# Kernel tuning notes

Hardware: AMD Instinct MI355X
Metric: run time of the kernel (lower is better)

## Reference

```python
import jax, jax.numpy as jnp
import numpy as np
from jax import lax

U, K, POOL, STRIDE, FC = 300, 19, 7, 7, 100   # num_units, filter size, maxpool, fc_size
B, L, D = 256, 1000, 4                        # batch, seq len, DNA dim
P = (L - (K - 1) - (POOL - 1) - 1) // STRIDE + 1  # post_pool_size = 140
EPS = 1e-5  # BatchNorm eps (eval mode with running stats; Dropout is identity in eval)


def setup_inputs() -> dict:
    key = jax.random.key(0)
    ks = jax.random.split(key, 24)
    rn = lambda k, shp, s=0.1: jax.random.normal(k, shp, jnp.float32) * s
    return {
        "input_seq": jax.random.normal(ks[0], (B, L, D), jnp.float32),
        # per-unit conv (groups=U on tiled input == plain Conv1d(4, U, K))
        "w_conv": rn(ks[1], (U, D, K)), "b_conv": rn(ks[2], (U,)),
        "g1": 1.0 + rn(ks[3], (U,)), "be1": rn(ks[4], (U,)),
        "m1": rn(ks[5], (U,)), "v1": 1.0 + jax.random.uniform(ks[6], (U,), jnp.float32),
        # per-unit FC1 (grouped 1x1 conv: P -> FC per unit)
        "w_fc1": rn(ks[7], (U, FC, P)), "b_fc1": rn(ks[8], (U, FC)),
        "g2": 1.0 + rn(ks[9], (U, FC)), "be2": rn(ks[10], (U, FC)),
        "m2": rn(ks[11], (U, FC)), "v2": 1.0 + jax.random.uniform(ks[12], (U, FC), jnp.float32),
        # per-unit FC2 (grouped 1x1 conv: FC -> 1 per unit)
        "w_fc2": rn(ks[13], (U, FC)), "b_fc2": rn(ks[14], (U,)),
        "g3": 1.0 + rn(ks[15], (U,)), "be3": rn(ks[16], (U,)),
        "m3": rn(ks[17], (U,)), "v3": 1.0 + jax.random.uniform(ks[18], (U,), jnp.float32),
        # final Linear(U, 1)
        "w_out": rn(ks[19], (U, 1)), "b_out": rn(ks[20], (1,)),
    }


def reference(input_seq, w_conv, b_conv, g1, be1, m1, v1, w_fc1, b_fc1,
              g2, be2, m2, v2, w_fc2, b_fc2, g3, be3, m3, v3, w_out, b_out):
    x = jnp.transpose(input_seq, (0, 2, 1))  # B,D,L
    # grouped conv on input tiled U times: every group sees the same D=4 channels,
    # so it is exactly a plain Conv1d(D, U, K).
    conv = lax.conv_general_dilated(
        x, w_conv, (1,), 'VALID', dimension_numbers=('NCH', 'OIH', 'NCH')
    ) + b_conv[None, :, None]                 # B,U,L' (L'=L-K+1)
    a = (conv - m1[None, :, None]) * (g1 / jnp.sqrt(v1 + EPS))[None, :, None] + be1[None, :, None]
    a = jnp.exp(a)
    pooled = lax.reduce_window(a, -jnp.inf, lax.max,
                               (1, 1, POOL), (1, 1, STRIDE), 'VALID')  # B,U,P
    # Flatten->Unsqueeze->grouped 1x1 conv == per-unit matmul over P
    h = jnp.einsum('bup,ufp->buf', pooled, w_fc1) + b_fc1               # B,U,FC
    h = jax.nn.relu((h - m2) * (g2 / jnp.sqrt(v2 + EPS)) + be2)
    z = jnp.einsum('buf,uf->bu', h, w_fc2) + b_fc2                      # B,U
    z = jax.nn.relu((z - m3) * (g3 / jnp.sqrt(v3 + EPS)) + be3)
    return jax.nn.sigmoid(z @ w_out + b_out)                            # B,1
```

## Files before the change

kernel.cpp:

```cpp
#include <hip/hip_runtime.h>
#include <hip/hip_bf16.h>
#include <math.h>

#define U_   300
#define K_   19
#define FC_  100
#define B_   256
#define L_   1000
#define P_   140
#define EPS_ 1e-5f
#define WLD_ 144

typedef unsigned short ushort_t;
typedef __attribute__((ext_vector_type(8)))  short short8v;
typedef __attribute__((ext_vector_type(16))) float f32x16;

__device__ __forceinline__ ushort_t f2bf(float f) {
    union { float f; unsigned u; } a; a.f = f;
    unsigned r = a.u + 0x7fffu + ((a.u >> 16) & 1u);
    return (ushort_t)(r >> 16);
}

__global__ __launch_bounds__(256, 4)
void pack_conv_k(const float* __restrict__ w_conv, const float* __restrict__ b_conv,
                 const float* __restrict__ g1, const float* __restrict__ be1,
                 const float* __restrict__ m1, const float* __restrict__ v1,
                 ushort_t* __restrict__ w_bf, float* __restrict__ o1g)
{
    const int t = blockIdx.x * 256 + threadIdx.x;
    if (t < 320 * 80) {
        const int u = t / 80, j = t - u * 80;
        float val = 0.f;
        if (u < U_ && j < 76) {
            const int tp = j >> 2;
            const int d  = j & 3;
            const float s1 = g1[u] / sqrtf(v1[u] + EPS_);
            val = w_conv[u * 76 + 19 * d + tp] * s1;
        }
        const int nt = u >> 5, r = u & 31;
        const int kc = j >> 4, rem = j & 15;
        const int half = rem >> 3, e = rem & 7;
        w_bf[nt * 2560 + kc * 512 + half * 256 + r * 8 + e] = f2bf(val);
    }
    if (t < 320) {
        float o = 0.f;
        if (t < U_) {
            const float s1 = g1[t] / sqrtf(v1[t] + EPS_);
            o = (b_conv[t] - m1[t]) * s1 + be1[t];
        }
        o1g[t] = o;
    }
}

__global__ __launch_bounds__(448, 4)
void conv_mfma_k(const float4* __restrict__ x4,
                 const ushort_t* __restrict__ w_bf,
                 const float* __restrict__ o1g,
                 ushort_t* __restrict__ pooled)
{
    __shared__ ushort_t xls[2][880];
    __shared__ ushort_t wlds[12800];
    __shared__ ushort_t stage[32][68];
    const int tid = threadIdx.x;
    const int bx  = blockIdx.x;
    const int nh  = blockIdx.y;
    const int b0  = 2 * blockIdx.z;
    const int w0  = bx * 28;
    const int l0  = w0 * 7;

    if (tid < 440) {
        const int which = (tid >= 220) ? 1 : 0;
        const int i = tid - 220 * which;
        const int gi = l0 + i;
        float4 v = make_float4(0.f, 0.f, 0.f, 0.f);
        if (gi < L_) v = x4[(size_t)(b0 + which) * L_ + gi];
        ushort4 pk4;
        pk4.x = f2bf(v.x); pk4.y = f2bf(v.y); pk4.z = f2bf(v.z); pk4.w = f2bf(v.w);
        *(ushort4*)&xls[which][4 * i] = pk4;
    }
    {
        const float4* ws = (const float4*)w_bf + nh * 1600;
        float4* wd = (float4*)wlds;
        for (int i = tid; i < 1600; i += 448) wd[i] = ws[i];
    }
    __syncthreads();

    const int lane = tid & 63;
    const int mt   = tid >> 6;
    const int half = lane >> 5;
    const int r32  = lane & 31;

    const int sreg = (r32 & 3) + 4 * (r32 >> 3);
    const int sh   = (r32 >> 2) & 1;
    const int off  = sreg < 7  ? sreg + 7 * sh
                   : sreg < 14 ? sreg + 7 + 7 * sh
                               : 28 + (sreg - 14) + 2 * sh;

    const char* xb0 = (const char*)&xls[0][0] + 8 * (28 * mt + off) + 16 * half;
    const char* xb1 = xb0 + 1760;
    const char* wl  = (const char*)wlds + 16 * lane;

    short8v aA0[5], aA1[5];
#pragma unroll
    for (int kc = 0; kc < 5; ++kc) {
        aA0[kc] = *(const short8v*)(xb0 + 32 * kc);
        aA1[kc] = *(const short8v*)(xb1 + 32 * kc);
    }

    const int dr  = tid / 7;
    const int dcc = tid - 7 * dr;
    const int dul = dr >> 1;
    const int dbl = dr & 1;

    const int p0off = 4 * mt + half;

    short8v bfr[5];
#pragma unroll
    for (int kc = 0; kc < 5; ++kc)
        bfr[kc] = *(const short8v*)(wl + kc * 1024);
    float o1u = o1g[nh * 160 + r32];

    for (int ntp = 0; ntp < 5; ++ntp) {
        const int ntn = (ntp < 4) ? ntp + 1 : ntp;
        short8v bnx[5];
#pragma unroll
        for (int kc = 0; kc < 5; ++kc)
            bnx[kc] = *(const short8v*)(wl + ntn * 5120 + kc * 1024);
        const float o1n = o1g[nh * 160 + ntn * 32 + r32];

        f32x16 acc0 = {};
        f32x16 acc1 = {};
#pragma unroll
        for (int kc = 0; kc < 5; ++kc) {
            acc0 = __builtin_amdgcn_mfma_f32_32x32x16_bf16(aA0[kc], bfr[kc], acc0, 0, 0, 0);
            acc1 = __builtin_amdgcn_mfma_f32_32x32x16_bf16(aA1[kc], bfr[kc], acc1, 0, 0, 0);
        }

        float m00 = acc0[0], m01 = acc0[7];
        float m10 = acc1[0], m11 = acc1[7];
#pragma unroll
        for (int j = 1; j < 7; ++j)  { m00 = fmaxf(m00, acc0[j]); m10 = fmaxf(m10, acc1[j]); }
#pragma unroll
        for (int j = 8; j < 14; ++j) { m01 = fmaxf(m01, acc0[j]); m11 = fmaxf(m11, acc1[j]); }

        stage[r32][p0off]          = f2bf(__expf(m00 + o1u));
        stage[r32][p0off + 2]      = f2bf(__expf(m01 + o1u));
        stage[r32][32 + p0off]     = f2bf(__expf(m10 + o1u));
        stage[r32][32 + p0off + 2] = f2bf(__expf(m11 + o1u));
        __syncthreads();

        const int ug = nh * 160 + ntp * 32 + dul;
        if (ug < U_) {
            const ushort4 st = *(const ushort4*)&stage[dul][dbl * 32 + 4 * dcc];
            *(ushort4*)&pooled[((size_t)ug * B_ + (b0 + dbl)) * P_ + w0 + 4 * dcc] = st;
        }
        __syncthreads();

#pragma unroll
        for (int kc = 0; kc < 5; ++kc) bfr[kc] = bnx[kc];
        o1u = o1n;
    }
}

__global__ __launch_bounds__(256, 3)
void fc_mfma_k(const ushort_t* __restrict__ pooled,
               const float* __restrict__ w_fc1,
               const float* __restrict__ b_fc1,
               const float* __restrict__ g2,
               const float* __restrict__ be2,
               const float* __restrict__ m2,
               const float* __restrict__ v2,
               const float* __restrict__ w_fc2,
               const float* __restrict__ b_fc2,
               const float* __restrict__ g3,
               const float* __restrict__ be3,
               const float* __restrict__ m3,
               const float* __restrict__ v3,
               float* __restrict__ zT)
{
    __shared__ ushort_t wlds[FC_ * WLD_];
    __shared__ float zred[128][33];
    const int tid  = threadIdx.x;
    const int bid = blockIdx.x;
    int u, bt;
    if (bid < 592) {
        const int r = bid & 7, k = bid >> 3;
        bt = k & 1;
        u  = (k >> 1) * 8 + r;
    } else {
        const int t = bid - 592;
        u  = 296 + (t >> 1);
        bt = t & 1;
    }

    const int lane = tid & 63;
    const int wv   = tid >> 6;
    const int half = lane >> 5;
    const int r32  = lane & 31;

    const int brow = bt * 128 + wv * 32 + r32;
    const ushort_t* __restrict__ abase =
        pooled + ((size_t)u * B_ + brow) * P_ + half * 8;
    short8v a[9];
#pragma unroll
    for (int kc = 0; kc < 9; ++kc)
        a[kc] = *(const short8v*)(abase + kc * 16);

    const float* __restrict__ wsrc = w_fc1 + (size_t)u * FC_ * P_;
    for (int idx = tid; idx < FC_ * 35; idx += 256) {
        const int f = idx / 35, j = idx - f * 35;
        const float4 v = *(const float4*)(wsrc + f * P_ + 4 * j);
        ushort4 pk;
        pk.x = f2bf(v.x); pk.y = f2bf(v.y); pk.z = f2bf(v.z); pk.w = f2bf(v.w);
        *(ushort4*)&wlds[f * WLD_ + 4 * j] = pk;
    }
    for (int idx = tid; idx < FC_ * 4; idx += 256) {
        const int f = idx >> 2, k = 140 + (idx & 3);
        wlds[f * WLD_ + k] = 0;
    }
    __syncthreads();

    const ushort_t* __restrict__ bl0 = &wlds[r32 * WLD_ + half * 8];
    const ushort_t* __restrict__ bl1 = &wlds[(32 + r32) * WLD_ + half * 8];
    const ushort_t* __restrict__ bl2 = &wlds[(64 + r32) * WLD_ + half * 8];
    const int f3c = (96 + r32 < FC_) ? (96 + r32) : (FC_ - 1);
    const ushort_t* __restrict__ bl3 = &wlds[f3c * WLD_ + half * 8];

    f32x16 acc0 = {}, acc1 = {}, acc2 = {}, acc3 = {};
#pragma unroll
    for (int kc = 0; kc < 9; ++kc) {
        const short8v b0 = *(const short8v*)(bl0 + kc * 16);
        const short8v b1 = *(const short8v*)(bl1 + kc * 16);
        const short8v b2 = *(const short8v*)(bl2 + kc * 16);
        const short8v b3 = *(const short8v*)(bl3 + kc * 16);
        acc0 = __builtin_amdgcn_mfma_f32_32x32x16_bf16(a[kc], b0, acc0, 0, 0, 0);
        acc1 = __builtin_amdgcn_mfma_f32_32x32x16_bf16(a[kc], b1, acc1, 0, 0, 0);
        acc2 = __builtin_amdgcn_mfma_f32_32x32x16_bf16(a[kc], b2, acc2, 0, 0, 0);
        acc3 = __builtin_amdgcn_mfma_f32_32x32x16_bf16(a[kc], b3, acc3, 0, 0, 0);
    }

    float s2[4], o2[4], w2[4];
#pragma unroll
    for (int n = 0; n < 4; ++n) {
        const int f = n * 32 + r32;
        if (f < FC_) {
            const int fg = u * FC_ + f;
            const float ss = g2[fg] / sqrtf(v2[fg] + EPS_);
            s2[n] = ss;
            o2[n] = (b_fc1[fg] - m2[fg]) * ss + be2[fg];
            w2[n] = w_fc2[fg];
        } else {
            s2[n] = 0.f; o2[n] = 0.f; w2[n] = 0.f;
        }
    }
#pragma unroll
    for (int rg = 0; rg < 16; ++rg) {
        const int row = (rg & 3) + 8 * (rg >> 2) + 4 * half;
        float s = fmaxf(fmaf(acc0[rg], s2[0], o2[0]), 0.f) * w2[0];
        s = fmaf(fmaxf(fmaf(acc1[rg], s2[1], o2[1]), 0.f), w2[1], s);
        s = fmaf(fmaxf(fmaf(acc2[rg], s2[2], o2[2]), 0.f), w2[2], s);
        s = fmaf(fmaxf(fmaf(acc3[rg], s2[3], o2[3]), 0.f), w2[3], s);
        zred[wv * 32 + row][r32] = s;
    }
    __syncthreads();

    if (tid < 128) {
        float s = 0.f;
#pragma unroll
        for (int j = 0; j < 32; ++j) s += zred[tid][j];
        const float s3 = g3[u] / sqrtf(v3[u] + EPS_);
        const float o3 = (b_fc2[u] - m3[u]) * s3 + be3[u];
        zT[(size_t)(bt * 128 + tid) * 304 + u] = fmaxf(fmaf(s, s3, o3), 0.f);
    }
}

__global__ __launch_bounds__(64, 8)
void out_k(const float* __restrict__ zT,
           const float* __restrict__ w_out,
           const float* __restrict__ b_out,
           float* __restrict__ out)
{
    const int lane = threadIdx.x;
    const int b    = blockIdx.x;
    const float4* zr = (const float4*)(zT + (size_t)b * 304);
    const float4* w4 = (const float4*)w_out;

    float s = 0.f;
    for (int i = lane; i < 75; i += 64) {
        const float4 z = zr[i], w = w4[i];
        s += z.x * w.x + z.y * w.y + z.z * w.z + z.w * w.w;
    }
#pragma unroll
    for (int o = 32; o > 0; o >>= 1) s += __shfl_xor(s, o);
    if (lane == 0)
        out[b] = 1.0f / (1.0f + __expf(-(s + b_out[0])));
}

extern "C" void kernel_launch(void* const* d_in, const int* in_sizes, int n_in,
                              void* d_out, int out_size, void* d_ws, size_t ws_size,
                              hipStream_t stream)
{
    const float* input_seq = (const float*)d_in[0];
    const float* w_conv    = (const float*)d_in[1];
    const float* b_conv    = (const float*)d_in[2];
    const float* g1        = (const float*)d_in[3];
    const float* be1       = (const float*)d_in[4];
    const float* m1        = (const float*)d_in[5];
    const float* v1        = (const float*)d_in[6];
    const float* w_fc1     = (const float*)d_in[7];
    const float* b_fc1     = (const float*)d_in[8];
    const float* g2        = (const float*)d_in[9];
    const float* be2       = (const float*)d_in[10];
    const float* m2        = (const float*)d_in[11];
    const float* v2        = (const float*)d_in[12];
    const float* w_fc2     = (const float*)d_in[13];
    const float* b_fc2     = (const float*)d_in[14];
    const float* g3        = (const float*)d_in[15];
    const float* be3       = (const float*)d_in[16];
    const float* m3        = (const float*)d_in[17];
    const float* v3        = (const float*)d_in[18];
    const float* w_out     = (const float*)d_in[19];
    const float* b_out     = (const float*)d_in[20];

    char* p = (char*)d_ws;
    ushort_t* pooled = (ushort_t*)p;   p += (size_t)B_ * U_ * P_ * 2;
    ushort_t* w_bf   = (ushort_t*)p;   p += 320 * 80 * 2;
    float*    o1g    = (float*)p;      p += 320 * 4;
    float*    zT     = (float*)p;      p += (size_t)B_ * 304 * 4;

    pack_conv_k<<<dim3(100), 256, 0, stream>>>(
        w_conv, b_conv, g1, be1, m1, v1, w_bf, o1g);

    conv_mfma_k<<<dim3(5, 2, 128), 448, 0, stream>>>(
        (const float4*)input_seq, w_bf, o1g, pooled);

    fc_mfma_k<<<dim3(600), 256, 0, stream>>>(
        pooled, w_fc1, b_fc1, g2, be2, m2, v2, w_fc2, b_fc2,
        g3, be3, m3, v3, zT);

    out_k<<<dim3(B_), 64, 0, stream>>>(zT, w_out, b_out, (float*)d_out);
}
```

Measured before the change: 55.77 us.

## Keep conv weights in registers and loop over batch pairs with double-buffered input

The conv kernel changes from staging a 160-unit weight slab in LDS and looping over five unit tiles to having each block hold one 32-unit weight tile in registers and loop over eight batch pairs. Input rows for the next batch pair are prefetched from global memory and written into a double-buffered LDS tile during the current iteration. This drops the large weight LDS copy and raises weight reuse per block, at the cost of fewer blocks overall and reloading input for each unit tile.

```diff
diff --git a/kernel.cpp b/kernel.cpp
--- a/kernel.cpp
+++ b/kernel.cpp
@@ -58,82 +58,77 @@
                  const float* __restrict__ o1g,
                  ushort_t* __restrict__ pooled)
 {
-    __shared__ ushort_t xls[2][880];
-    __shared__ ushort_t wlds[12800];
+    __shared__ ushort_t xls[2][2][880];
     __shared__ ushort_t stage[32][68];
     const int tid = threadIdx.x;
     const int bx  = blockIdx.x;
-    const int nh  = blockIdx.y;
-    const int b0  = 2 * blockIdx.z;
+    const int nt  = blockIdx.y;
+    const int pg  = blockIdx.z;
     const int w0  = bx * 28;
     const int l0  = w0 * 7;
-
-    if (tid < 440) {
-        const int which = (tid >= 220) ? 1 : 0;
-        const int i = tid - 220 * which;
-        const int gi = l0 + i;
-        float4 v = make_float4(0.f, 0.f, 0.f, 0.f);
-        if (gi < L_) v = x4[(size_t)(b0 + which) * L_ + gi];
-        ushort4 pk4;
-        pk4.x = f2bf(v.x); pk4.y = f2bf(v.y); pk4.z = f2bf(v.z); pk4.w = f2bf(v.w);
-        *(ushort4*)&xls[which][4 * i] = pk4;
-    }
-    {
-        const float4* ws = (const float4*)w_bf + nh * 1600;
-        float4* wd = (float4*)wlds;
-        for (int i = tid; i < 1600; i += 448) wd[i] = ws[i];
-    }
-    __syncthreads();
 
     const int lane = tid & 63;
     const int mt   = tid >> 6;
     const int half = lane >> 5;
     const int r32  = lane & 31;
+
+    const char* wgl = (const char*)w_bf + nt * 5120 + 16 * lane;
+    short8v Bf[5];
+#pragma unroll
+    for (int kc = 0; kc < 5; ++kc)
+        Bf[kc] = *(const short8v*)(wgl + kc * 1024);
+    const float o1u = o1g[nt * 32 + r32];
+
+    const int swhich = (tid >= 220) ? 1 : 0;
+    const int srow   = tid - 220 * swhich;
+    const int gi     = l0 + srow;
+
+    {
+        const int b00 = 2 * (pg * 8);
+        if (tid < 440) {
+            float4 v = make_float4(0.f, 0.f, 0.f, 0.f);
+            if (gi < L_) v = x4[(size_t)(b00 + swhich) * L_ + gi];
+            ushort4 pk4;
+            pk4.x = f2bf(v.x); pk4.y = f2bf(v.y); pk4.z = f2bf(v.z); pk4.w = f2bf(v.w);
+            *(ushort4*)&xls[0][swhich][4 * srow] = pk4;
+        }
+    }
+    __syncthreads();
 
     const int sreg = (r32 & 3) + 4 * (r32 >> 3);
     const int sh   = (r32 >> 2) & 1;
     const int off  = sreg < 7  ? sreg + 7 * sh
                    : sreg < 14 ? sreg + 7 + 7 * sh
                                : 28 + (sreg - 14) + 2 * sh;
-
-    const char* xb0 = (const char*)&xls[0][0] + 8 * (28 * mt + off) + 16 * half;
-    const char* xb1 = xb0 + 1760;
-    const char* wl  = (const char*)wlds + 16 * lane;
-
-    short8v aA0[5], aA1[5];
-#pragma unroll
-    for (int kc = 0; kc < 5; ++kc) {
-        aA0[kc] = *(const short8v*)(xb0 + 32 * kc);
-        aA1[kc] = *(const short8v*)(xb1 + 32 * kc);
-    }
+    const int xoffb = 8 * (28 * mt + off) + 16 * half;
 
     const int dr  = tid / 7;
     const int dcc = tid - 7 * dr;
     const int dul = dr >> 1;
     const int dbl = dr & 1;
+    const int ug  = nt * 32 + dul;
+    const bool dok = (ug < U_);
 
     const int p0off = 4 * mt + half;
 
-    short8v bfr[5];
-#pragma unroll
-    for (int kc = 0; kc < 5; ++kc)
-        bfr[kc] = *(const short8v*)(wl + kc * 1024);
-    float o1u = o1g[nh * 160 + r32];
-
-    for (int ntp = 0; ntp < 5; ++ntp) {
-        const int ntn = (ntp < 4) ? ntp + 1 : ntp;
-        short8v bnx[5];
-#pragma unroll
-        for (int kc = 0; kc < 5; ++kc)
-            bnx[kc] = *(const short8v*)(wl + ntn * 5120 + kc * 1024);
-        const float o1n = o1g[nh * 160 + ntn * 32 + r32];
+    for (int p = 0; p < 8; ++p) {
+        const int b0 = 2 * (pg * 8 + p);
+
+        float4 vnx = make_float4(0.f, 0.f, 0.f, 0.f);
+        if (p < 7 && tid < 440 && gi < L_)
+            vnx = x4[(size_t)(b0 + 2 + swhich) * L_ + gi];
+
+        const char* xb0 = (const char*)&xls[p & 1][0][0] + xoffb;
+        const char* xb1 = xb0 + 1760;
 
         f32x16 acc0 = {};
         f32x16 acc1 = {};
 #pragma unroll
         for (int kc = 0; kc < 5; ++kc) {
-            acc0 = __builtin_amdgcn_mfma_f32_32x32x16_bf16(aA0[kc], bfr[kc], acc0, 0, 0, 0);
-            acc1 = __builtin_amdgcn_mfma_f32_32x32x16_bf16(aA1[kc], bfr[kc], acc1, 0, 0, 0);
+            const short8v a0 = *(const short8v*)(xb0 + 32 * kc);
+            const short8v a1 = *(const short8v*)(xb1 + 32 * kc);
+            acc0 = __builtin_amdgcn_mfma_f32_32x32x16_bf16(a0, Bf[kc], acc0, 0, 0, 0);
+            acc1 = __builtin_amdgcn_mfma_f32_32x32x16_bf16(a1, Bf[kc], acc1, 0, 0, 0);
         }
 
         float m00 = acc0[0], m01 = acc0[7];
@@ -149,16 +144,17 @@
         stage[r32][32 + p0off + 2] = f2bf(__expf(m11 + o1u));
         __syncthreads();
 
-        const int ug = nh * 160 + ntp * 32 + dul;
-        if (ug < U_) {
+        if (dok) {
             const ushort4 st = *(const ushort4*)&stage[dul][dbl * 32 + 4 * dcc];
             *(ushort4*)&pooled[((size_t)ug * B_ + (b0 + dbl)) * P_ + w0 + 4 * dcc] = st;
         }
+
+        if (p < 7 && tid < 440) {
+            ushort4 pk4;
+            pk4.x = f2bf(vnx.x); pk4.y = f2bf(vnx.y); pk4.z = f2bf(vnx.z); pk4.w = f2bf(vnx.w);
+            *(ushort4*)&xls[(p + 1) & 1][swhich][4 * srow] = pk4;
+        }
         __syncthreads();
-
-#pragma unroll
-        for (int kc = 0; kc < 5; ++kc) bfr[kc] = bnx[kc];
-        o1u = o1n;
     }
 }
 
@@ -331,7 +327,7 @@
     pack_conv_k<<<dim3(100), 256, 0, stream>>>(
         w_conv, b_conv, g1, be1, m1, v1, w_bf, o1g);
 
-    conv_mfma_k<<<dim3(5, 2, 128), 448, 0, stream>>>(
+    conv_mfma_k<<<dim3(5, 10, 16), 448, 0, stream>>>(
         (const float4*)input_seq, w_bf, o1g, pooled);
 
     fc_mfma_k<<<dim3(600), 256, 0, stream>>>(
```

New measurement: 98.05 us. 1.76x slower.
